# Kernel optimization log

Hardware: AMD Instinct MI355X
Metric: run time of the kernel (lower is better)

Reference implementation:

```python
import jax, jax.numpy as jnp
import numpy as np

DIM = 1536
NHEADS = 12
HEADDIM = DIM // NHEADS  # 128
F, H, W = 5, 26, 30
S = F * H * W  # 3900
MAXPOS = 1024
EPS = 1e-6


def setup_inputs() -> dict:
    key = jax.random.key(0)
    ks = jax.random.split(key, 6)
    x = jax.random.normal(ks[0], (1, S, DIM), jnp.float32)
    seq_lens = jnp.array([S], jnp.int32)
    grid_sizes = jnp.array([[F, H, W]], jnp.int32)
    # complex RoPE table as (cos, sin) pairs: [1024, head_dim//2, 2]
    c = HEADDIM // 2
    inv = 1.0 / (10000.0 ** (np.arange(c, dtype=np.float64) / c))
    theta = np.arange(MAXPOS, dtype=np.float64)[:, None] * inv[None, :]
    freqs = jnp.asarray(np.stack([np.cos(theta), np.sin(theta)], axis=-1), jnp.float32)
    scale = 1.0 / np.sqrt(DIM)
    Wq = jax.random.normal(ks[1], (DIM, DIM), jnp.float32) * scale
    Wk = jax.random.normal(ks[2], (DIM, DIM), jnp.float32) * scale
    Wv = jax.random.normal(ks[3], (DIM, DIM), jnp.float32) * scale
    Wo = jax.random.normal(ks[4], (DIM, DIM), jnp.float32) * scale
    bq = jnp.zeros((DIM,), jnp.float32)
    bk = jnp.zeros((DIM,), jnp.float32)
    bv = jnp.zeros((DIM,), jnp.float32)
    bo = jnp.zeros((DIM,), jnp.float32)
    gq = jnp.ones((DIM,), jnp.float32)
    gk = jnp.ones((DIM,), jnp.float32)
    return dict(x=x, seq_lens=seq_lens, grid_sizes=grid_sizes, freqs=freqs,
                Wq=Wq, bq=bq, Wk=Wk, bk=bk, Wv=Wv, bv=bv, Wo=Wo, bo=bo, gq=gq, gk=gk)


def _rms_norm(z, g):
    zf = z.astype(jnp.float32)
    y = zf * jax.lax.rsqrt(jnp.mean(zf * zf, axis=-1, keepdims=True) + EPS)
    return y.astype(z.dtype) * g


def _build_freqs_i(freqs_c, f, h, w):
    # freqs_c: complex [1024, c]; split c into [c-2*(c//3), c//3, c//3] for (F,H,W)
    c = freqs_c.shape[1]
    c3 = c // 3
    c0 = c - 2 * c3
    ff = jnp.broadcast_to(freqs_c[:f, :c0][:, None, None, :], (f, h, w, c0))
    fh = jnp.broadcast_to(freqs_c[:h, c0:c0 + c3][None, :, None, :], (f, h, w, c3))
    fw = jnp.broadcast_to(freqs_c[:w, c0 + c3:][None, None, :, :], (f, h, w, c3))
    return jnp.concatenate([ff, fh, fw], axis=-1).reshape(f * h * w, 1, c)


def _rope_apply(t, freqs_i):
    # t: [1, S, n, d]; interpret last dim as c complex pairs and rotate
    b, s, n, d = t.shape
    c = d // 2
    t2 = t[0].reshape(s, n, c, 2)
    tc = jax.lax.complex(t2[..., 0], t2[..., 1])  # [S, n, c]
    tc = tc * freqs_i  # broadcast [S, 1, c]
    out = jnp.stack([jnp.real(tc), jnp.imag(tc)], axis=-1).reshape(s, n, d)
    return out[None].astype(jnp.float32)


def reference(x, seq_lens, grid_sizes, freqs, Wq, bq, Wk, bk, Wv, bv, Wo, bo, gq, gk):
    b, s, dim = x.shape
    d = freqs.shape[1] * 2  # head_dim
    n = dim // d
    q = _rms_norm(x @ Wq + bq, gq).reshape(b, s, n, d)
    k = _rms_norm(x @ Wk + bk, gk).reshape(b, s, n, d)
    v = (x @ Wv + bv).reshape(b, s, n, d)
    f, h, w = [int(t) for t in np.asarray(grid_sizes)[0]]
    freqs_c = jax.lax.complex(freqs[..., 0], freqs[..., 1])  # [1024, c]
    freqs_i = _build_freqs_i(freqs_c, f, h, w)  # [S, 1, c]
    q = _rope_apply(q, freqs_i)
    k = _rope_apply(k, freqs_i)
    # scaled dot-product attention with key-length mask
    scale = 1.0 / jnp.sqrt(jnp.asarray(d, jnp.float32))
    scores = jnp.einsum('bqnd,bknd->bnqk', q, k) * scale  # [1, n, S, S]
    key_mask = (jnp.arange(s)[None, None, None, :] < seq_lens[:, None, None, None])
    scores = jnp.where(key_mask, scores, jnp.asarray(-1e30, scores.dtype))
    attn = jax.nn.softmax(scores, axis=-1)
    out = jnp.einsum('bnqk,bknd->bqnd', attn, v)  # [1, S, n, d]
    out = out.reshape(b, s, dim)
    return out @ Wo + bo
```

## Files before the change

kernel.cpp:

```cpp
#include <hip/hip_runtime.h>
#include <stdint.h>

#define DIM 1536
#define SLEN 3900
#define SPAD 3904
#define NH 12
#define HD 128
#define SKP 136
#define SVP 68
#define KSPLIT 1984

typedef __bf16 bf16x8 __attribute__((ext_vector_type(8)));
typedef float f32x4 __attribute__((ext_vector_type(4)));

__device__ __forceinline__ float b2f(uint16_t u) {
  union { uint32_t i; float f; } x; x.i = ((uint32_t)u) << 16; return x.f;
}
__device__ __forceinline__ uint16_t f2b(float f) {
  union { __bf16 h; uint16_t u; } c; c.h = (__bf16)f; return c.u;
}
__device__ __forceinline__ bf16x8 ld8bf(const uint16_t* p) {
  bf16x8 r; __builtin_memcpy(&r, p, 16); return r;
}
__device__ __forceinline__ void st8(uint16_t* p, bf16x8 v) {
  __builtin_memcpy(p, &v, 16);
}
__device__ __forceinline__ void gl_lds16(const void* g, void* l) {
  __builtin_amdgcn_global_load_lds((__attribute__((address_space(1))) void*)(g),
                                   (__attribute__((address_space(3))) void*)(l),
                                   16, 0, 0);
}
__device__ __forceinline__ uint16_t* swz256(uint16_t* b, int row, int ce) {
  return (uint16_t*)((char*)b + row * 256 + ((ce * 2) ^ ((row & 7) << 4)));
}
__device__ __forceinline__ uint16_t* swz128(uint16_t* b, int row, int ce) {
  return (uint16_t*)((char*)b + row * 128 + ((ce * 2) ^ ((row & 7) << 4)));
}

__global__ __launch_bounds__(256) void conv_x(
    const float* __restrict__ x, uint16_t* __restrict__ xb) {
  int i = (blockIdx.x * 256 + threadIdx.x) * 8;
  float a[8];
  __builtin_memcpy(a, x + i, 32);
  uint16_t t[8];
#pragma unroll
  for (int q = 0; q < 8; q++) t[q] = f2b(a[q]);
  __builtin_memcpy(xb + i, t, 16);
}

__global__ __launch_bounds__(256) void transposeW4(
    const float* __restrict__ w0, const float* __restrict__ w1,
    const float* __restrict__ w2, const float* __restrict__ w3,
    uint16_t* __restrict__ WT4) {
  __shared__ uint16_t t[32][33];
  const int z = blockIdx.z;
  const float* src = z == 0 ? w0 : z == 1 ? w1 : z == 2 ? w2 : w3;
  uint16_t* dst = WT4 + (size_t)z * DIM * DIM;
  const int bx = blockIdx.x * 32, by = blockIdx.y * 32;
  const int tx = threadIdx.x & 31, ty = threadIdx.x >> 5;
#pragma unroll
  for (int i = 0; i < 32; i += 8)
    t[ty + i][tx] = f2b(src[(size_t)(by + ty + i) * DIM + bx + tx]);
  __syncthreads();
#pragma unroll
  for (int i = 0; i < 32; i += 8)
    dst[(size_t)(bx + ty + i) * DIM + by + tx] = t[tx][ty + i];
}

__global__ __launch_bounds__(256) void gemm(
    const uint16_t* __restrict__ A, const uint16_t* __restrict__ BT4,
    uint16_t* __restrict__ Cb, float* __restrict__ Cf,
    const float* __restrict__ bias, int M, int mode) {
  __shared__ __align__(16) uint16_t sA[128 * 32];
  __shared__ __align__(16) uint16_t sB[128 * 32];
  const int z = blockIdx.z;
  const uint16_t* BT = BT4 + (size_t)z * DIM * DIM;
  const int m0 = blockIdx.x * 128;
  const int n0 = blockIdx.y * 128;
  const int tid = threadIdx.x;
  const int wave = tid >> 6, lane = tid & 63;
  const int mh = (wave >> 1) * 64, nh = (wave & 1) * 64;
  const int lr = lane >> 2, lc = (lane & 3) * 8;
  const int r0 = wave * 32;
  const int fm = mh + (lane & 15);
  const int fn = nh + (lane & 15);
  const int ko = (lane >> 4) * 8;

  f32x4 acc[4][4];
  const f32x4 z4 = {0.f, 0.f, 0.f, 0.f};
#pragma unroll
  for (int i = 0; i < 4; i++)
#pragma unroll
    for (int j = 0; j < 4; j++) acc[i][j] = z4;

  for (int k0 = 0; k0 < DIM; k0 += 32) {
    __syncthreads();
#pragma unroll
    for (int j = 0; j < 2; j++) {
      int ra = m0 + r0 + j * 16 + lr; ra = ra < M ? ra : M - 1;
      gl_lds16(A + (size_t)ra * DIM + k0 + lc, (char*)sA + (r0 + j * 16) * 64);
      int rb = n0 + r0 + j * 16 + lr;
      gl_lds16(BT + (size_t)rb * DIM + k0 + lc, (char*)sB + (r0 + j * 16) * 64);
    }
    __builtin_amdgcn_s_waitcnt(0x0f70);
    __syncthreads();
    bf16x8 fa[4], fb[4];
#pragma unroll
    for (int i = 0; i < 4; i++) {
      fa[i] = ld8bf(sA + (fm + i * 16) * 32 + ko);
      fb[i] = ld8bf(sB + (fn + i * 16) * 32 + ko);
    }
#pragma unroll
    for (int i = 0; i < 4; i++)
#pragma unroll
      for (int j = 0; j < 4; j++)
        acc[i][j] = __builtin_amdgcn_mfma_f32_16x16x32_bf16(fa[i], fb[j], acc[i][j], 0, 0, 0);
  }
#pragma unroll
  for (int j = 0; j < 4; j++) {
    int col = n0 + nh + j * 16 + (lane & 15);
    float bvv = (mode == 0 && bias) ? bias[col] : 0.f;
#pragma unroll
    for (int i = 0; i < 4; i++) {
      int row = m0 + mh + i * 16 + (lane >> 4) * 4;
#pragma unroll
      for (int r = 0; r < 4; r++) {
        if (row + r < M) {
          float val = acc[i][j][r] + bvv;
          if (mode == 0)
            Cf[(size_t)(row + r) * DIM + col] = val;
          else
            Cb[(size_t)z * ((size_t)NH * SLEN * HD) +
               (size_t)(col >> 7) * ((size_t)SLEN * HD) +
               (size_t)(row + r) * HD + (col & 127)] = f2b(val);
        }
      }
    }
  }
}

__global__ __launch_bounds__(256) void norm_rope(
    uint16_t* __restrict__ Qb, uint16_t* __restrict__ Kb,
    const float* __restrict__ bq, const float* __restrict__ bk,
    const float* __restrict__ gq, const float* __restrict__ gk,
    const float* __restrict__ freqs, const int* __restrict__ gsz) {
  const int s = blockIdx.x;
  const int isK = blockIdx.y;
  uint32_t* B = (uint32_t*)(isK ? Kb : Qb);
  const float2* br = (const float2*)(isK ? bk : bq);
  const float2* gr = (const float2*)(isK ? gk : gq);
  const int tid = threadIdx.x;
  float va[3], vb[3];
  float ss = 0.f;
#pragma unroll
  for (int i = 0; i < 3; i++) {
    int p = tid + i * 256;
    int h = p >> 6, j = p & 63;
    size_t a = (size_t)h * (SLEN * 64) + (size_t)s * 64 + j;
    uint32_t u = B[a];
    float2 ub = br[p];
    float x0 = b2f((uint16_t)(u & 0xffff)) + ub.x;
    float x1 = b2f((uint16_t)(u >> 16)) + ub.y;
    va[i] = x0; vb[i] = x1; ss += x0 * x0 + x1 * x1;
  }
#pragma unroll
  for (int o = 32; o > 0; o >>= 1) ss += __shfl_down(ss, o, 64);
  __shared__ float red[4];
  if ((tid & 63) == 0) red[tid >> 6] = ss;
  __syncthreads();
  ss = red[0] + red[1] + red[2] + red[3];
  float rr = rsqrtf(ss * (1.0f / DIM) + 1e-6f);
  if (!isK) rr *= 0.08838834764831845f * 1.4426950408889634f;
  const int H = gsz[1], W = gsz[2];
  const int hw = H * W;
  const int fi = s / hw, rem = s - fi * hw;
  const int hi = rem / W, wi = rem - hi * W;
#pragma unroll
  for (int i = 0; i < 3; i++) {
    int p = tid + i * 256;
    int h = p >> 6, j = p & 63;
    int prow = (j < 22) ? fi : (j < 43) ? hi : wi;
    float2 f2 = ((const float2*)freqs)[prow * 64 + j];
    float2 g2 = gr[p];
    float na = va[i] * rr * g2.x;
    float nb = vb[i] * rr * g2.y;
    float ra = na * f2.x - nb * f2.y;
    float rb = na * f2.y + nb * f2.x;
    size_t a = (size_t)h * (SLEN * 64) + (size_t)s * 64 + j;
    B[a] = (uint32_t)f2b(ra) | ((uint32_t)f2b(rb) << 16);
  }
}

__global__ __launch_bounds__(256) void v_reformat(
    const uint16_t* __restrict__ Vb, const float* __restrict__ bv,
    uint16_t* __restrict__ VT) {
  __shared__ uint16_t t[128][136];
  const int head = blockIdx.x;
  const int s0 = blockIdx.y * 128;
  const int tid = threadIdx.x;
  const int cb = (tid & 15) * 8, rb = tid >> 4;
  const uint16_t* Vh = Vb + (size_t)head * SLEN * HD;
  float bvf[8];
#pragma unroll
  for (int q = 0; q < 8; q++) bvf[q] = bv[head * HD + cb + q];
#pragma unroll
  for (int pass = 0; pass < 8; pass++) {
    int r = rb + pass * 16;
    int s = s0 + r; int sc = s < SLEN ? s : SLEN - 1;
    uint16_t u[8];
    __builtin_memcpy(u, Vh + (size_t)sc * HD + cb, 16);
#pragma unroll
    for (int q = 0; q < 8; q++) t[r][cb + q] = f2b(b2f(u[q]) + bvf[q]);
  }
  __syncthreads();
  const int sb = (tid & 15) * 8, db = tid >> 4;
#pragma unroll
  for (int pass = 0; pass < 8; pass++) {
    int d = db + pass * 16;
    uint16_t out[8] __attribute__((aligned(16)));
#pragma unroll
    for (int i2 = 0; i2 < 8; i2++) {
      int s = s0 + sb + i2;
      out[i2] = (s < SLEN) ? t[sb + i2][d] : (uint16_t)0;
    }
    size_t base = ((size_t)head * HD + d) * SPAD + s0 + sb;
    if (s0 + sb + 8 <= SLEN) {
      __builtin_memcpy(VT + base, out, 16);
    } else {
#pragma unroll
      for (int i2 = 0; i2 < 8; i2++) {
        int s = s0 + sb + i2;
        if (s < SPAD) VT[base + i2] = out[i2];
      }
    }
  }
}

__global__ __launch_bounds__(256) void attn_split(
    const uint16_t* __restrict__ Q, const uint16_t* __restrict__ K,
    const uint16_t* __restrict__ VT, float* __restrict__ Op,
    float* __restrict__ Lp, const int* __restrict__ seq_lens) {
  __shared__ __align__(16) uint16_t sK[64 * 128];
  __shared__ __align__(16) uint16_t sV[128 * 64];
  __shared__ __align__(16) uint16_t sP[128 * 64];
  const int head = blockIdx.x;
  const int q0 = blockIdx.y * 128;
  const int zz = blockIdx.z;
  const int kvbeg = zz ? KSPLIT : 0;
  const int kvend = zz ? SLEN : KSPLIT;
  const int tid = threadIdx.x;
  const int wave = tid >> 6, lane = tid & 63;
  int sl = seq_lens[0];
  const int seqlen = sl < SLEN ? sl : SLEN;
  const uint16_t* Qh = Q + (size_t)head * SLEN * HD;
  const uint16_t* Kh = K + (size_t)head * SLEN * HD;
  const uint16_t* Vh = VT + (size_t)head * HD * SPAD;

  const int fm = lane & 15;
  const int ko = (lane >> 4) * 8;
  const int kr0 = tid >> 4, kcc = (tid & 15) * 8;
  const int vd0 = tid >> 3, vcc = (tid & 7) * 8;

  bf16x8 aq[2][4];
#pragma unroll
  for (int half = 0; half < 2; half++) {
#pragma unroll
    for (int ps = 0; ps < 4; ps++) {
      int row = kr0 + ps * 16;
      int qg = q0 + half * 64 + row; qg = qg < SLEN ? qg : SLEN - 1;
      st8(swz256(sK, row, kcc), ld8bf(Qh + (size_t)qg * HD + kcc));
    }
    __syncthreads();
#pragma unroll
    for (int kc = 0; kc < 4; kc++)
      aq[half][kc] = ld8bf(swz256(sK, wave * 16 + fm, kc * 32 + ko));
    __syncthreads();
  }

  f32x4 o[2][8];
  const f32x4 z4 = {0.f, 0.f, 0.f, 0.f};
#pragma unroll
  for (int h2 = 0; h2 < 2; h2++)
#pragma unroll
    for (int j = 0; j < 8; j++) o[h2][j] = z4;
  float l_r[2][4] = {{0.f, 0.f, 0.f, 0.f}, {0.f, 0.f, 0.f, 0.f}};

  bf16x8 kr[4], vr[4];
#pragma unroll
  for (int ps = 0; ps < 4; ps++) {
    kr[ps] = ld8bf(Kh + (size_t)(kvbeg + kr0 + ps * 16) * HD + kcc);
    vr[ps] = ld8bf(Vh + (size_t)(vd0 + ps * 32) * SPAD + kvbeg + vcc);
  }

  for (int kv0 = kvbeg; kv0 < kvend; kv0 += 64) {
    __syncthreads();
#pragma unroll
    for (int ps = 0; ps < 4; ps++) {
      st8(swz256(sK, kr0 + ps * 16, kcc), kr[ps]);
      st8(swz128(sV, vd0 + ps * 32, vcc), vr[ps]);
    }
    __syncthreads();
    int nv0 = kv0 + 64;
    if (nv0 < kvend) {
#pragma unroll
      for (int ps = 0; ps < 4; ps++) {
        int kg = nv0 + kr0 + ps * 16; kg = kg < SLEN ? kg : SLEN - 1;
        kr[ps] = ld8bf(Kh + (size_t)kg * HD + kcc);
        vr[ps] = ld8bf(Vh + (size_t)(vd0 + ps * 32) * SPAD + nv0 + vcc);
      }
    }

    f32x4 sc[2][4];
#pragma unroll
    for (int h2 = 0; h2 < 2; h2++)
#pragma unroll
      for (int kk = 0; kk < 4; kk++) sc[h2][kk] = z4;
    __builtin_amdgcn_s_setprio(1);
#pragma unroll
    for (int kc = 0; kc < 4; kc++) {
#pragma unroll
      for (int kk = 0; kk < 4; kk++) {
        bf16x8 bkf = ld8bf(swz256(sK, kk * 16 + fm, kc * 32 + ko));
        sc[0][kk] = __builtin_amdgcn_mfma_f32_16x16x32_bf16(aq[0][kc], bkf, sc[0][kk], 0, 0, 0);
        sc[1][kk] = __builtin_amdgcn_mfma_f32_16x16x32_bf16(aq[1][kc], bkf, sc[1][kk], 0, 0, 0);
      }
    }
    __builtin_amdgcn_s_setprio(0);
#pragma unroll
    for (int h2 = 0; h2 < 2; h2++) {
#pragma unroll
      for (int kk = 0; kk < 4; kk++) {
        int col = kv0 + kk * 16 + fm;
        bool valid = col < seqlen;
#pragma unroll
        for (int r = 0; r < 4; r++) {
          float p = valid ? exp2f(sc[h2][kk][r]) : 0.f;
          l_r[h2][r] += p;
          *swz128(sP, h2 * 64 + wave * 16 + (lane >> 4) * 4 + r, kk * 16 + fm) = f2b(p);
        }
      }
    }
    __builtin_amdgcn_s_setprio(1);
#pragma unroll
    for (int kc = 0; kc < 2; kc++) {
      bf16x8 ap0 = ld8bf(swz128(sP, wave * 16 + fm, kc * 32 + ko));
      bf16x8 ap1 = ld8bf(swz128(sP, 64 + wave * 16 + fm, kc * 32 + ko));
#pragma unroll
      for (int j = 0; j < 8; j++) {
        bf16x8 bvf = ld8bf(swz128(sV, j * 16 + fm, kc * 32 + ko));
        o[0][j] = __builtin_amdgcn_mfma_f32_16x16x32_bf16(ap0, bvf, o[0][j], 0, 0, 0);
        o[1][j] = __builtin_amdgcn_mfma_f32_16x16x32_bf16(ap1, bvf, o[1][j], 0, 0, 0);
      }
    }
    __builtin_amdgcn_s_setprio(0);
  }
#pragma unroll
  for (int h2 = 0; h2 < 2; h2++)
#pragma unroll
    for (int r = 0; r < 4; r++) {
#pragma unroll
      for (int off = 1; off < 16; off <<= 1)
        l_r[h2][r] += __shfl_xor(l_r[h2][r], off, 64);
    }
  float* Oz = Op + (size_t)zz * ((size_t)SLEN * DIM);
#pragma unroll
  for (int h2 = 0; h2 < 2; h2++) {
#pragma unroll
    for (int r = 0; r < 4; r++) {
      int row = q0 + h2 * 64 + wave * 16 + (lane >> 4) * 4 + r;
      if (row < SLEN) {
#pragma unroll
        for (int j = 0; j < 8; j++) {
          int col = head * HD + j * 16 + fm;
          Oz[(size_t)row * DIM + col] = o[h2][j][r];
        }
        if (fm == 0) Lp[((size_t)zz * NH + head) * SLEN + row] = l_r[h2][r];
      }
    }
  }
}

__global__ __launch_bounds__(256) void combine(
    const float* __restrict__ Op, const float* __restrict__ Lp,
    uint16_t* __restrict__ AO) {
  int i = (blockIdx.x * 256 + threadIdx.x) * 8;
  int row = i / DIM;
  int col = i - row * DIM;
  int head = col >> 7;
  float l = Lp[(size_t)head * SLEN + row] + Lp[(size_t)(NH + head) * SLEN + row];
  float inv = 1.0f / l;
  float a[8], b[8];
  __builtin_memcpy(a, Op + i, 32);
  __builtin_memcpy(b, Op + (size_t)SLEN * DIM + i, 32);
  uint16_t t[8];
#pragma unroll
  for (int q = 0; q < 8; q++) t[q] = f2b((a[q] + b[q]) * inv);
  __builtin_memcpy(AO + i, t, 16);
}

__global__ __launch_bounds__(256) void attn(
    const uint16_t* __restrict__ Q, const uint16_t* __restrict__ K,
    const uint16_t* __restrict__ VT, uint16_t* __restrict__ O,
    const int* __restrict__ seq_lens) {
  __shared__ __align__(16) uint16_t sK[64 * SKP];
  __shared__ __align__(16) uint16_t sV[128 * SVP];
  __shared__ __align__(16) uint16_t sP[64 * SVP];
  const int head = blockIdx.x;
  const int q0 = blockIdx.y * 64;
  const int tid = threadIdx.x;
  const int wave = tid >> 6, lane = tid & 63;
  int sl = seq_lens[0];
  const int seqlen = sl < SLEN ? sl : SLEN;
  const uint16_t* Qh = Q + (size_t)head * SLEN * HD;
  const uint16_t* Kh = K + (size_t)head * SLEN * HD;
  const uint16_t* Vh = VT + (size_t)head * HD * SPAD;
  const int fm = lane & 15;
  const int ko = (lane >> 4) * 8;
  const int kr0 = tid >> 4, kcc = (tid & 15) * 8;
  const int vd0 = tid >> 3, vcc = (tid & 7) * 8;
#pragma unroll
  for (int ps = 0; ps < 4; ps++) {
    int row = kr0 + ps * 16;
    int qg = q0 + row; qg = qg < SLEN ? qg : SLEN - 1;
    st8(sK + row * SKP + kcc, ld8bf(Qh + (size_t)qg * HD + kcc));
  }
  __syncthreads();
  bf16x8 aq[4];
#pragma unroll
  for (int kc = 0; kc < 4; kc++)
    aq[kc] = ld8bf(sK + (wave * 16 + fm) * SKP + kc * 32 + ko);
  f32x4 o[8];
  const f32x4 z4 = {0.f, 0.f, 0.f, 0.f};
#pragma unroll
  for (int j = 0; j < 8; j++) o[j] = z4;
  float l_r[4] = {0.f, 0.f, 0.f, 0.f};
  bf16x8 kr[4], vr[4];
#pragma unroll
  for (int ps = 0; ps < 4; ps++) {
    kr[ps] = ld8bf(Kh + (size_t)(kr0 + ps * 16) * HD + kcc);
    vr[ps] = ld8bf(Vh + (size_t)(vd0 + ps * 32) * SPAD + vcc);
  }
  for (int kv0 = 0; kv0 < SLEN; kv0 += 64) {
    __syncthreads();
#pragma unroll
    for (int ps = 0; ps < 4; ps++) {
      st8(sK + (kr0 + ps * 16) * SKP + kcc, kr[ps]);
      st8(sV + (vd0 + ps * 32) * SVP + vcc, vr[ps]);
    }
    __syncthreads();
    int nv0 = kv0 + 64;
    if (nv0 < SLEN) {
#pragma unroll
      for (int ps = 0; ps < 4; ps++) {
        int kg = nv0 + kr0 + ps * 16; kg = kg < SLEN ? kg : SLEN - 1;
        kr[ps] = ld8bf(Kh + (size_t)kg * HD + kcc);
        vr[ps] = ld8bf(Vh + (size_t)(vd0 + ps * 32) * SPAD + nv0 + vcc);
      }
    }
    f32x4 sc[4];
#pragma unroll
    for (int kk = 0; kk < 4; kk++) sc[kk] = z4;
    __builtin_amdgcn_s_setprio(1);
#pragma unroll
    for (int kc = 0; kc < 4; kc++) {
#pragma unroll
      for (int kk = 0; kk < 4; kk++) {
        bf16x8 bkf = ld8bf(sK + (kk * 16 + fm) * SKP + kc * 32 + ko);
        sc[kk] = __builtin_amdgcn_mfma_f32_16x16x32_bf16(aq[kc], bkf, sc[kk], 0, 0, 0);
      }
    }
    __builtin_amdgcn_s_setprio(0);
#pragma unroll
    for (int kk = 0; kk < 4; kk++) {
      int col = kv0 + kk * 16 + fm;
      bool valid = col < seqlen;
#pragma unroll
      for (int r = 0; r < 4; r++) {
        float p = valid ? exp2f(sc[kk][r]) : 0.f;
        l_r[r] += p;
        sP[(wave * 16 + (lane >> 4) * 4 + r) * SVP + kk * 16 + fm] = f2b(p);
      }
    }
    __builtin_amdgcn_s_setprio(1);
#pragma unroll
    for (int kc = 0; kc < 2; kc++) {
      bf16x8 ap = ld8bf(sP + (wave * 16 + fm) * SVP + kc * 32 + ko);
#pragma unroll
      for (int j = 0; j < 8; j++) {
        bf16x8 bvf = ld8bf(sV + (j * 16 + fm) * SVP + kc * 32 + ko);
        o[j] = __builtin_amdgcn_mfma_f32_16x16x32_bf16(ap, bvf, o[j], 0, 0, 0);
      }
    }
    __builtin_amdgcn_s_setprio(0);
  }
#pragma unroll
  for (int r = 0; r < 4; r++) {
#pragma unroll
    for (int off = 1; off < 16; off <<= 1) l_r[r] += __shfl_xor(l_r[r], off, 64);
  }
#pragma unroll
  for (int r = 0; r < 4; r++) {
    int row = q0 + wave * 16 + (lane >> 4) * 4 + r;
    if (row < SLEN) {
      float inv = 1.0f / l_r[r];
#pragma unroll
      for (int j = 0; j < 8; j++) {
        int col = head * HD + j * 16 + fm;
        O[(size_t)row * DIM + col] = f2b(o[j][r] * inv);
      }
    }
  }
}

extern "C" void kernel_launch(void* const* d_in, const int* in_sizes, int n_in,
                              void* d_out, int out_size, void* d_ws, size_t ws_size,
                              hipStream_t stream) {
  const float* x      = (const float*)d_in[0];
  const int* seq_lens = (const int*)d_in[1];
  const int* gsz      = (const int*)d_in[2];
  const float* freqs  = (const float*)d_in[3];
  const float* Wq     = (const float*)d_in[4];
  const float* bq     = (const float*)d_in[5];
  const float* Wk     = (const float*)d_in[6];
  const float* bk     = (const float*)d_in[7];
  const float* Wv     = (const float*)d_in[8];
  const float* bv     = (const float*)d_in[9];
  const float* Wo     = (const float*)d_in[10];
  const float* bo     = (const float*)d_in[11];
  const float* gq     = (const float*)d_in[12];
  const float* gk     = (const float*)d_in[13];

  char* p = (char*)d_ws;
  uint16_t* WT4 = (uint16_t*)p; p += (size_t)4 * DIM * DIM * 2;
  uint16_t* Qb  = (uint16_t*)p; p += (size_t)NH * SLEN * HD * 2;
  uint16_t* Kb  = (uint16_t*)p; p += (size_t)NH * SLEN * HD * 2;
  uint16_t* Vb  = (uint16_t*)p; p += (size_t)NH * SLEN * HD * 2;
  uint16_t* VTb = (uint16_t*)p; p += (size_t)NH * HD * SPAD * 2;
  float*    Opb = (float*)p;    p += (size_t)2 * SLEN * DIM * 4;
  float*    Lpb = (float*)p;    p += (size_t)2 * NH * SLEN * 4;
  const size_t need = (size_t)(p - (char*)d_ws);
  uint16_t* xb  = VTb;
  uint16_t* AO  = Vb;

  conv_x<<<dim3(2925), 256, 0, stream>>>(x, xb);
  transposeW4<<<dim3(48, 48, 4), 256, 0, stream>>>(Wq, Wk, Wv, Wo, WT4);

  gemm<<<dim3(31, 12, 3), 256, 0, stream>>>(xb, WT4, Qb, nullptr, nullptr, SLEN, 1);

  norm_rope<<<dim3(SLEN, 2), 256, 0, stream>>>(Qb, Kb, bq, bk, gq, gk, freqs, gsz);
  v_reformat<<<dim3(NH, 31), 256, 0, stream>>>(Vb, bv, VTb);

  if (ws_size >= need) {
    attn_split<<<dim3(NH, 31, 2), 256, 0, stream>>>(Qb, Kb, VTb, Opb, Lpb, seq_lens);
    combine<<<dim3(2925), 256, 0, stream>>>(Opb, Lpb, AO);
  } else {
    attn<<<dim3(NH, 61), 256, 0, stream>>>(Qb, Kb, VTb, AO, seq_lens);
  }

  gemm<<<dim3(31, 12, 1), 256, 0, stream>>>(AO, WT4 + (size_t)3 * DIM * DIM,
                                            nullptr, (float*)d_out, bo, SLEN, 0);
}
```

Before: 517.8 us.

## Load K/V tiles directly to LDS and interleave QK MFMA with softmax

Replaces the register-staged prefetch of K and V (global→VGPR→LDS with one-tile lookahead) with direct global-to-LDS loads, using an XOR pre-swizzled source address to match the LDS swizzle layout. Each iteration now issues the loads, waits on vmcnt, then syncs. The QK score loop is reordered per 16-column chunk so exp and P stores follow each chunk's MFMAs, which lowers live score registers. The cost is losing the software prefetch overlap, since loads are now waited on immediately, in exchange for fewer VGPRs and fewer LDS store instructions.

```diff
diff --git a/kernel.cpp b/kernel.cpp
--- a/kernel.cpp
+++ b/kernel.cpp
@@ -259,7 +259,8 @@
   const int fm = lane & 15;
   const int ko = (lane >> 4) * 8;
   const int kr0 = tid >> 4, kcc = (tid & 15) * 8;
-  const int vd0 = tid >> 3, vcc = (tid & 7) * 8;
+  const int kselb = (((tid & 15) ^ ((tid >> 4) & 7)) << 4);
+  const int vselb = (((tid & 7) ^ ((tid >> 3) & 7)) << 4);
 
   bf16x8 aq[2][4];
 #pragma unroll
@@ -285,59 +286,41 @@
     for (int j = 0; j < 8; j++) o[h2][j] = z4;
   float l_r[2][4] = {{0.f, 0.f, 0.f, 0.f}, {0.f, 0.f, 0.f, 0.f}};
 
-  bf16x8 kr[4], vr[4];
-#pragma unroll
-  for (int ps = 0; ps < 4; ps++) {
-    kr[ps] = ld8bf(Kh + (size_t)(kvbeg + kr0 + ps * 16) * HD + kcc);
-    vr[ps] = ld8bf(Vh + (size_t)(vd0 + ps * 32) * SPAD + kvbeg + vcc);
-  }
-
   for (int kv0 = kvbeg; kv0 < kvend; kv0 += 64) {
     __syncthreads();
 #pragma unroll
     for (int ps = 0; ps < 4; ps++) {
-      st8(swz256(sK, kr0 + ps * 16, kcc), kr[ps]);
-      st8(swz128(sV, vd0 + ps * 32, vcc), vr[ps]);
-    }
-    __syncthreads();
-    int nv0 = kv0 + 64;
-    if (nv0 < kvend) {
-#pragma unroll
-      for (int ps = 0; ps < 4; ps++) {
-        int kg = nv0 + kr0 + ps * 16; kg = kg < SLEN ? kg : SLEN - 1;
-        kr[ps] = ld8bf(Kh + (size_t)kg * HD + kcc);
-        vr[ps] = ld8bf(Vh + (size_t)(vd0 + ps * 32) * SPAD + nv0 + vcc);
-      }
-    }
-
-    f32x4 sc[2][4];
-#pragma unroll
-    for (int h2 = 0; h2 < 2; h2++)
-#pragma unroll
-      for (int kk = 0; kk < 4; kk++) sc[h2][kk] = z4;
-    __builtin_amdgcn_s_setprio(1);
-#pragma unroll
-    for (int kc = 0; kc < 4; kc++) {
-#pragma unroll
-      for (int kk = 0; kk < 4; kk++) {
+      int kg = kv0 + ps * 16 + (tid >> 4); kg = kg < SLEN ? kg : SLEN - 1;
+      gl_lds16((const char*)Kh + (size_t)kg * 256 + kselb,
+               (char*)sK + ps * 4096 + wave * 1024);
+      int d = ps * 32 + (tid >> 3);
+      gl_lds16((const char*)Vh + (size_t)d * (SPAD * 2) + (size_t)kv0 * 2 + vselb,
+               (char*)sV + ps * 4096 + wave * 1024);
+    }
+    __builtin_amdgcn_s_waitcnt(0x0f70);
+    __syncthreads();
+
+#pragma unroll
+    for (int kk = 0; kk < 4; kk++) {
+      f32x4 s0 = z4, s1 = z4;
+      __builtin_amdgcn_s_setprio(1);
+#pragma unroll
+      for (int kc = 0; kc < 4; kc++) {
         bf16x8 bkf = ld8bf(swz256(sK, kk * 16 + fm, kc * 32 + ko));
-        sc[0][kk] = __builtin_amdgcn_mfma_f32_16x16x32_bf16(aq[0][kc], bkf, sc[0][kk], 0, 0, 0);
-        sc[1][kk] = __builtin_amdgcn_mfma_f32_16x16x32_bf16(aq[1][kc], bkf, sc[1][kk], 0, 0, 0);
-      }
-    }
-    __builtin_amdgcn_s_setprio(0);
-#pragma unroll
-    for (int h2 = 0; h2 < 2; h2++) {
-#pragma unroll
-      for (int kk = 0; kk < 4; kk++) {
-        int col = kv0 + kk * 16 + fm;
-        bool valid = col < seqlen;
-#pragma unroll
-        for (int r = 0; r < 4; r++) {
-          float p = valid ? exp2f(sc[h2][kk][r]) : 0.f;
-          l_r[h2][r] += p;
-          *swz128(sP, h2 * 64 + wave * 16 + (lane >> 4) * 4 + r, kk * 16 + fm) = f2b(p);
-        }
+        s0 = __builtin_amdgcn_mfma_f32_16x16x32_bf16(aq[0][kc], bkf, s0, 0, 0, 0);
+        s1 = __builtin_amdgcn_mfma_f32_16x16x32_bf16(aq[1][kc], bkf, s1, 0, 0, 0);
+      }
+      __builtin_amdgcn_s_setprio(0);
+      int col = kv0 + kk * 16 + fm;
+      bool valid = col < seqlen;
+#pragma unroll
+      for (int r = 0; r < 4; r++) {
+        float p0 = valid ? exp2f(s0[r]) : 0.f;
+        float p1 = valid ? exp2f(s1[r]) : 0.f;
+        l_r[0][r] += p0;
+        l_r[1][r] += p1;
+        *swz128(sP, wave * 16 + (lane >> 4) * 4 + r, kk * 16 + fm) = f2b(p0);
+        *swz128(sP, 64 + wave * 16 + (lane >> 4) * 4 + r, kk * 16 + fm) = f2b(p1);
       }
     }
     __builtin_amdgcn_s_setprio(1);
```

After: 466.1 us. 1.11x faster.
